# Optimization experiments

Measured on AMD Instinct MI355X. Metric: run time of the kernel, lower is better.

## Reference

```python
import jax, jax.numpy as jnp
import numpy as np

T, B, D, H, R, S, M = 1024, 16, 512, 8, 32, 16, 16
TQ = R + T + S   # query length
KL = M + R + T   # key/value length
NEG_INF = -1e8


def setup_inputs() -> dict:
    key = jax.random.key(0)
    ks = jax.random.split(key, 12)
    utterance = jax.random.normal(ks[0], (T, B, D), jnp.float32)
    right_context = jax.random.normal(ks[1], (R, B, D), jnp.float32)
    summary = jax.random.normal(ks[2], (S, B, D), jnp.float32)
    mems = jax.random.normal(ks[3], (M, B, D), jnp.float32)
    # valid lengths in [T//2, T]; force max == T so data-dependent shapes are static
    lengths = jax.random.randint(ks[4], (B,), T // 2, T + 1).at[0].set(T).astype(jnp.int64)
    # block-streaming style mask: query i may only attend to keys <= i + M
    q_idx = jnp.arange(TQ)[:, None]
    k_idx = jnp.arange(KL)[None, :]
    attention_mask = k_idx > (q_idx + M)  # True = masked
    scale = 0.02
    Wq = jax.random.normal(ks[5], (D, D), jnp.float32) * scale
    bq = jnp.zeros((D,), jnp.float32)
    Wkv = jax.random.normal(ks[6], (2 * D, D), jnp.float32) * scale
    bkv = jnp.zeros((2 * D,), jnp.float32)
    Wo = jax.random.normal(ks[7], (D, D), jnp.float32) * scale
    bo = jnp.zeros((D,), jnp.float32)
    return dict(utterance=utterance, lengths=lengths, right_context=right_context,
                summary=summary, mems=mems, attention_mask=attention_mask,
                Wq=Wq, bq=bq, Wkv=Wkv, bkv=bkv, Wo=Wo, bo=bo)


def _split_heads(x):
    # (L, B, D) -> (B*H, L, D//H), matching torch .view(-1, B*H, d).transpose(0, 1)
    L = x.shape[0]
    return x.reshape(L, B * H, D // H).transpose(1, 0, 2)


def reference(utterance, lengths, right_context, summary, mems, attention_mask,
              Wq, bq, Wkv, bkv, Wo, bo):
    d_head = D // H
    scaling = d_head ** -0.5

    query_in = jnp.concatenate([right_context, utterance, summary], axis=0)   # (TQ, B, D)
    kv_in = jnp.concatenate([mems, right_context, utterance], axis=0)         # (KL, B, D)

    query = query_in @ Wq.T + bq
    kv = kv_in @ Wkv.T + bkv
    k, v = jnp.split(kv, 2, axis=2)

    q = _split_heads(query)  # (B*H, TQ, d)
    kh = _split_heads(k)     # (B*H, KL, d)
    vh = _split_heads(v)

    w = jnp.einsum('nqd,nkd->nqk', q * scaling, kh).astype(jnp.float32)
    w = jnp.where(attention_mask[None, :, :], NEG_INF, w)

    # padding mask (B > 1 path): klengths = lengths + M + right_context_blocks_length
    rcbl = TQ - jnp.max(lengths) - S  # == R since max(lengths) == T
    klengths = lengths + M + rcbl
    pad_mask = jnp.arange(KL)[None, :] >= klengths[:, None]  # (B, KL)
    w = w.reshape(B, H, TQ, KL)
    w = jnp.where(pad_mask[:, None, None, :], NEG_INF, w)
    w = w.reshape(B * H, TQ, KL)

    probs = jax.nn.softmax(w, axis=-1)  # dropout p=0.0
    attn = jnp.einsum('nqk,nkd->nqd', probs, vh)          # (B*H, TQ, d)
    attn = attn.transpose(1, 0, 2).reshape(TQ, B, D)

    out = attn @ Wo.T + bo                                # (TQ, B, D)
    output_right_context = out[:TQ - S]                    # (R+T, B, D)
    output_mems = jnp.clip(out[TQ - S:], -10.0, 10.0)      # tanh_on_mem=False
    return output_right_context, output_mems[:-1]          # (S-1, B, D)
```

## Files before the change

### kernel.cpp

```cpp
#include <hip/hip_runtime.h>

#define T_   1024
#define B_   16
#define D_   512
#define H_   8
#define R_   32
#define S_   16
#define M_   16
#define TQ_  1072
#define KL_  1072
#define DH_  64
#define NROW 17152
#define K_   512
#define LQ_  268
#define QSCALE 0.18033688f

typedef unsigned short u16;
using bf16x8 = __attribute__((ext_vector_type(8))) short;
using f32x4  = __attribute__((ext_vector_type(4))) float;
using u16x4  = __attribute__((ext_vector_type(4))) unsigned short;

__device__ __forceinline__ u16 f2bf(float f) {
    unsigned int u = __builtin_bit_cast(unsigned int, f);
    unsigned int r = u + 0x7fffu + ((u >> 16) & 1u);
    return (u16)(r >> 16);
}

__device__ __forceinline__ unsigned int cvt_pk_bf16(float a, float b) {
    unsigned int r;
    asm("v_cvt_pk_bf16_f32 %0, %1, %2" : "=v"(r) : "v"(a), "v"(b));
    return r;
}

__device__ __forceinline__ void gload_lds16(const u16* g, u16* l) {
    __builtin_amdgcn_global_load_lds(
        (const __attribute__((address_space(1))) unsigned int*)g,
        (__attribute__((address_space(3))) unsigned int*)l,
        16, 0, 0);
}

__global__ void k_convert4(const float4* __restrict__ utt, const float4* __restrict__ rc,
                           const float4* __restrict__ smr, const float4* __restrict__ mems,
                           const float4* __restrict__ Wq, const float4* __restrict__ Wkv,
                           const float4* __restrict__ Wo,
                           u16x4* __restrict__ xall,
                           u16x4* __restrict__ wq, u16x4* __restrict__ wkv,
                           u16x4* __restrict__ wo)
{
    const int N4 = 17408 * D_ / 4;
    const int MB = M_ * B_ * D_ / 4;
    const int RB = MB + R_ * B_ * D_ / 4;
    const int UB = RB + T_ * B_ * D_ / 4;
    const int W1 = D_ * D_ / 4, W2 = 2 * D_ * D_ / 4;
    for (int i = blockIdx.x * blockDim.x + threadIdx.x; i < N4;
         i += gridDim.x * blockDim.x) {
        float4 v;
        if (i < MB)      v = mems[i];
        else if (i < RB) v = rc[i - MB];
        else if (i < UB) v = utt[i - RB];
        else             v = smr[i - UB];
        xall[i] = (u16x4){f2bf(v.x), f2bf(v.y), f2bf(v.z), f2bf(v.w)};
        if (i < W1) { v = Wq[i];  wq[i]  = (u16x4){f2bf(v.x), f2bf(v.y), f2bf(v.z), f2bf(v.w)}; }
        if (i < W2) { v = Wkv[i]; wkv[i] = (u16x4){f2bf(v.x), f2bf(v.y), f2bf(v.z), f2bf(v.w)}; }
        if (i < W1) { v = Wo[i];  wo[i]  = (u16x4){f2bf(v.x), f2bf(v.y), f2bf(v.z), f2bf(v.w)}; }
    }
}

template<int MREP, bool TOR>
__device__ __forceinline__ void pipe_core(const u16* __restrict__ Ab,
                                          const u16* __restrict__ Wb,
                                          u16* lds, f32x4* acc)
{
    const int BM = MREP * 32;
    u16* As0 = lds;
    u16* As1 = lds + BM * 64;
    u16* Bs0 = lds + 2 * BM * 64;
    u16* Bs1 = lds + 2 * BM * 64 + 256 * 64;

    const int tid  = threadIdx.x;
    const int wid  = tid >> 6, lane = tid & 63;
    const int wm   = wid >> 2, wn = wid & 3;
    const int col  = lane & 15, quad = lane >> 4;
    const int sr   = tid >> 3;
    const int sc   = (tid & 7) ^ (sr & 7);
    const u16* gA  = Ab + (size_t)sr * K_ + sc * 8;
    const u16* gB  = Wb + (size_t)sr * K_ + sc * 8;

#pragma unroll
    for (int i = 0; i < MREP * 4; i++) acc[i] = (f32x4){0.f, 0.f, 0.f, 0.f};

    auto stage = [&](int kt, u16* Au, u16* Bu) {
#pragma unroll
        for (int i = 0; i < MREP / 2; i++)
            gload_lds16(gA + (size_t)(i * 64) * K_ + kt * 64,
                        Au + (i * 64 + wid * 8) * 64);
#pragma unroll
        for (int i = 0; i < 4; i++)
            gload_lds16(gB + (size_t)(i * 64) * K_ + kt * 64,
                        Bu + (i * 64 + wid * 8) * 64);
    };

    stage(0, As0, Bs0);
    __syncthreads();

    u16 *Ac = As0, *Bc = Bs0, *An = As1, *Bn = Bs1;
    for (int kt = 0; kt < 8; ++kt) {
        if (kt < 7) stage(kt + 1, An, Bn);
#pragma unroll
        for (int kh = 0; kh < 2; ++kh) {
            bf16x8 aF[MREP], bF[4];
#pragma unroll
            for (int mi = 0; mi < MREP; mi++)
                aF[mi] = *(const bf16x8*)&Ac[(wm * (MREP * 16) + mi * 16 + col) * 64
                             + (((kh * 4 + quad) ^ (col & 7)) * 8)];
#pragma unroll
            for (int ni = 0; ni < 4; ni++)
                bF[ni] = *(const bf16x8*)&Bc[(wn * 64 + ni * 16 + col) * 64
                             + (((kh * 4 + quad) ^ (col & 7)) * 8)];
            __builtin_amdgcn_s_setprio(1);
            if (TOR) {
#pragma unroll
                for (int ni = 0; ni < 4; ni++)
#pragma unroll
                    for (int mi = 0; mi < MREP; mi++)
                        acc[ni * MREP + mi] = __builtin_amdgcn_mfma_f32_16x16x32_bf16(
                            bF[ni], aF[mi], acc[ni * MREP + mi], 0, 0, 0);
            } else {
#pragma unroll
                for (int mi = 0; mi < MREP; mi++)
#pragma unroll
                    for (int ni = 0; ni < 4; ni++)
                        acc[mi * 4 + ni] = __builtin_amdgcn_mfma_f32_16x16x32_bf16(
                            aF[mi], bF[ni], acc[mi * 4 + ni], 0, 0, 0);
            }
            __builtin_amdgcn_s_setprio(0);
        }
        __syncthreads();
        u16* t;
        t = Ac; Ac = An; An = t;
        t = Bc; Bc = Bn; Bn = t;
    }
}

__global__ __launch_bounds__(512, 2)
void k_gemm_qkv8(const u16* __restrict__ xall,
                 const u16* __restrict__ wqp, const u16* __restrict__ wkvp,
                 const float* __restrict__ bq, const float* __restrict__ bkv,
                 u16* __restrict__ qb, u16* __restrict__ kb, u16* __restrict__ vt)
{
    extern __shared__ u16 lds[];
    const int bid = blockIdx.x;
    const int tn = bid % 6, tm = bid / 6;
    const int typ = tn >> 1, half = tn & 1;
    const u16* Ab = (typ == 0 ? xall + (size_t)256 * K_ : xall)
                    + (size_t)tm * 256 * K_;
    const u16* Wb = (typ == 0 ? wqp : wkvp + (typ == 2 ? (size_t)512 * K_ : 0))
                    + (size_t)half * 256 * K_;

    const int wid = threadIdx.x >> 6, lane = threadIdx.x & 63;
    const int wm = wid >> 2, wn = wid & 3;
    const int col = lane & 15, quad = lane >> 4;

    f32x4 acc[32];
    if (typ == 2) {
        pipe_core<8, false>(Ab, Wb, lds, acc);
#pragma unroll
        for (int ni = 0; ni < 4; ni++) {
            const int f = half * 256 + wn * 64 + ni * 16 + col;
            const float bs = bkv[512 + f];
#pragma unroll
            for (int mg = 0; mg < 2; mg++) {
                const int lq = tm * 4 + wm * 2 + mg;
#pragma unroll
                for (int r = 0; r < 4; r++) {
                    const int bb = quad * 4 + r;
                    uint2 pk;
                    pk.x = cvt_pk_bf16(acc[(mg * 4 + 0) * 4 + ni][r] + bs,
                                       acc[(mg * 4 + 1) * 4 + ni][r] + bs);
                    pk.y = cvt_pk_bf16(acc[(mg * 4 + 2) * 4 + ni][r] + bs,
                                       acc[(mg * 4 + 3) * 4 + ni][r] + bs);
                    *(uint2*)&vt[(((size_t)bb * LQ_ + lq) * 512 + f) * 4] = pk;
                }
            }
        }
    } else {
        pipe_core<8, true>(Ab, Wb, lds, acc);
        const float* bias = (typ == 0) ? bq : bkv;
        u16* outp = (typ == 0) ? qb : kb;
        const float qs = (typ == 0) ? QSCALE : 1.0f;
#pragma unroll
        for (int ni = 0; ni < 4; ni++) {
            const int gc0 = half * 256 + wn * 64 + ni * 16 + quad * 4;
            const float4 bs4 = *(const float4*)&bias[gc0];
#pragma unroll
            for (int mi = 0; mi < 8; mi++) {
                const int mrow = tm * 256 + wm * 128 + mi * 16 + col;
                f32x4 a = acc[ni * 8 + mi];
                uint2 pk;
                pk.x = cvt_pk_bf16((a[0] + bs4.x) * qs, (a[1] + bs4.y) * qs);
                pk.y = cvt_pk_bf16((a[2] + bs4.z) * qs, (a[3] + bs4.w) * qs);
                *(uint2*)&outp[(size_t)mrow * 512 + gc0] = pk;
            }
        }
    }
}

__global__ __launch_bounds__(512, 2)
void k_gemm_o8(const u16* __restrict__ A, const u16* __restrict__ W,
               const float* __restrict__ bias, float* __restrict__ Co)
{
    extern __shared__ u16 lds[];
    const int tn = blockIdx.x % 2, tm = blockIdx.x / 2;
    const u16* Ab = A + (size_t)tm * 128 * K_;
    const u16* Wb = W + (size_t)tn * 256 * K_;

    const int wid = threadIdx.x >> 6, lane = threadIdx.x & 63;
    const int wm = wid >> 2, wn = wid & 3;
    const int col = lane & 15, quad = lane >> 4;

    f32x4 acc[16];
    pipe_core<4, true>(Ab, Wb, lds, acc);

#pragma unroll
    for (int ni = 0; ni < 4; ni++) {
        const int gc0 = tn * 256 + wn * 64 + ni * 16 + quad * 4;
        const float4 bs4 = *(const float4*)&bias[gc0];
#pragma unroll
        for (int mi = 0; mi < 4; mi++) {
            const int l = tm * 8 + wm * 4 + mi;
            if (l == TQ_ - 1) continue;
            const int mrow = tm * 128 + wm * 64 + mi * 16 + col;
            f32x4 a = acc[ni * 4 + mi];
            float4 v = {a[0] + bs4.x, a[1] + bs4.y, a[2] + bs4.z, a[3] + bs4.w};
            if (l >= TQ_ - S_) {
                v.x = fminf(10.0f, fmaxf(-10.0f, v.x));
                v.y = fminf(10.0f, fmaxf(-10.0f, v.y));
                v.z = fminf(10.0f, fmaxf(-10.0f, v.z));
                v.w = fminf(10.0f, fmaxf(-10.0f, v.w));
            }
            *(float4*)&Co[(size_t)mrow * 512 + gc0] = v;
        }
    }
}

__global__ __launch_bounds__(256, 2)
void k_attn5(const u16* __restrict__ qbuf, const u16* __restrict__ kb,
             const u16* __restrict__ vt, const int* __restrict__ lenp,
             u16* __restrict__ attnb)
{
    __shared__ __align__(16) u16 Ks[2][64 * 64];
    __shared__ __align__(16) u16 Vs[2][64 * 64];
    __shared__ __align__(16) u16 Ps[4][16 * 64];

    const int blk  = blockIdx.x;
    const int qblk = 16 - (blk >> 7);
    const int bh   = blk & 127;
    const int b = bh >> 3, h = bh & 7;
    const int tid = threadIdx.x;
    const int w = tid >> 6, lane = tid & 63;
    const int col = lane & 15, quad = lane >> 4;

    int stride = (lenp[1] == 0) ? 2 : 1;
    int maxlen = 0;
    for (int i = 0; i < B_; i++) maxlen = max(maxlen, lenp[i * stride]);
    const int klen = lenp[b * stride] + M_ + (TQ_ - maxlen - S_);

    const int q0 = qblk * 64;
    const int qw = q0 + w * 16;
    const int q  = qw + col;

    int qrow = min(q, TQ_ - 1);
    const u16* qp = qbuf + ((size_t)qrow * B_ + b) * D_ + h * DH_ + quad * 8;
    bf16x8 bq0 = *(const bf16x8*)(qp);
    bf16x8 bq1 = *(const bf16x8*)(qp + 32);

    const int s0 = tid, s1 = tid + 256;
    const u16* kbase = kb + (size_t)b * 512 + h * DH_;
    size_t kof0 = (size_t)(s0 >> 3) * 8192 + (size_t)(((s0 & 7) ^ ((s0 >> 3) & 7)) * 8);
    size_t kof1 = (size_t)(s1 >> 3) * 8192 + (size_t)(((s1 & 7) ^ ((s1 >> 3) & 7)) * 8);
    const u16* vbase = vt + ((size_t)b * LQ_ * 512 + (size_t)h * DH_) * 4;
    auto vchunk = [](int s) -> size_t {
        int fp = s >> 4;
        int lq = (s & 15) ^ (fp & 15);
        return (size_t)lq * 2048 + (size_t)fp * 8;
    };
    const size_t vof0 = vchunk(s0), vof1 = vchunk(s1);

    float li = 0.f;
    f32x4 o[4];
#pragma unroll
    for (int g = 0; g < 4; g++) o[g] = (f32x4){0.f, 0.f, 0.f, 0.f};

    const int nk = min(q0 + 64 + M_, klen);
    const int numkt = (nk + 63) >> 6;
    u16* pw = &Ps[w][0];

    gload_lds16(kbase + kof0, &Ks[0][(size_t)w * 512]);
    gload_lds16(kbase + kof1, &Ks[0][2048 + (size_t)w * 512]);
    gload_lds16(vbase + vof0, &Vs[0][(size_t)w * 512]);
    gload_lds16(vbase + vof1, &Vs[0][2048 + (size_t)w * 512]);

    for (int kt = 0; kt < numkt; kt++) {
        const int kn0 = kt * 64;
        const int cur = kt & 1;
        __syncthreads();
        if (kt + 1 < numkt) {
            const size_t kstep = (size_t)(kn0 + 64) * 8192;
            const size_t vstep = (size_t)(kt + 1) * 32768;
            gload_lds16(kbase + kstep + kof0, &Ks[cur ^ 1][(size_t)w * 512]);
            gload_lds16(kbase + kstep + kof1, &Ks[cur ^ 1][2048 + (size_t)w * 512]);
            gload_lds16(vbase + vstep + vof0, &Vs[cur ^ 1][(size_t)w * 512]);
            gload_lds16(vbase + vstep + vof1, &Vs[cur ^ 1][2048 + (size_t)w * 512]);
        }

        f32x4 sc[4];
        __builtin_amdgcn_s_setprio(1);
#pragma unroll
        for (int g = 0; g < 4; g++) {
            int key = g * 16 + col;
            bf16x8 a0 = *(const bf16x8*)&Ks[cur][key * 64 + ((quad ^ (key & 7)) * 8)];
            bf16x8 a1 = *(const bf16x8*)&Ks[cur][key * 64 + (((4 + quad) ^ (key & 7)) * 8)];
            f32x4 z = {0.f, 0.f, 0.f, 0.f};
            z = __builtin_amdgcn_mfma_f32_16x16x32_bf16(a0, bq0, z, 0, 0, 0);
            z = __builtin_amdgcn_mfma_f32_16x16x32_bf16(a1, bq1, z, 0, 0, 0);
            sc[g] = z;
        }
        __builtin_amdgcn_s_setprio(0);

        const bool needmask = (kn0 + 63 > qw + M_) || (kn0 + 63 >= klen);
        if (needmask) {
#pragma unroll
            for (int g = 0; g < 4; g++)
#pragma unroll
                for (int r = 0; r < 4; r++) {
                    int key = kn0 + g * 16 + quad * 4 + r;
                    bool valid = (key <= q + M_) && (key < klen);
                    sc[g][r] = valid ? sc[g][r] : -1e8f;
                }
        }

#pragma unroll
        for (int g = 0; g < 4; g++) {
            float pr[4];
#pragma unroll
            for (int r = 0; r < 4; r++) {
                pr[r] = __builtin_amdgcn_exp2f(sc[g][r]);
                li += pr[r];
            }
            uint2 pk;
            pk.x = cvt_pk_bf16(pr[0], pr[1]);
            pk.y = cvt_pk_bf16(pr[2], pr[3]);
            int kc = g * 2 + (quad >> 1);
            *(uint2*)&pw[col * 64 + ((kc ^ (col & 7)) * 8) + (quad & 1) * 4] = pk;
        }

        bf16x8 ap0 = *(const bf16x8*)&pw[col * 64 + ((quad ^ (col & 7)) * 8)];
        bf16x8 ap1 = *(const bf16x8*)&pw[col * 64 + (((4 + quad) ^ (col & 7)) * 8)];
        __builtin_amdgcn_s_setprio(1);
#pragma unroll
        for (int g = 0; g < 4; g++) {
            int d = g * 16 + col;
            int fp = d >> 1, fo = (d & 1) * 4;
            bf16x8 bv[2];
#pragma unroll
            for (int hh = 0; hh < 2; hh++) {
                int lqA = hh * 8 + quad * 2;
                int posA = fp * 16 + (lqA ^ (fp & 15));
                int posB = fp * 16 + ((lqA + 1) ^ (fp & 15));
                u16x4 loA = *(const u16x4*)&Vs[cur][posA * 8 + fo];
                u16x4 loB = *(const u16x4*)&Vs[cur][posB * 8 + fo];
                bf16x8 t;
                t[0] = loA[0]; t[1] = loA[1]; t[2] = loA[2]; t[3] = loA[3];
                t[4] = loB[0]; t[5] = loB[1]; t[6] = loB[2]; t[7] = loB[3];
                bv[hh] = t;
            }
            o[g] = __builtin_amdgcn_mfma_f32_16x16x32_bf16(bv[0], ap0, o[g], 0, 0, 0);
            o[g] = __builtin_amdgcn_mfma_f32_16x16x32_bf16(bv[1], ap1, o[g], 0, 0, 0);
        }
        __builtin_amdgcn_s_setprio(0);
    }

    li += __shfl_xor(li, 16);
    li += __shfl_xor(li, 32);
    const float inv = 1.0f / li;
    const int qo = qw + col;
    if (qw + 16 <= TQ_) {
#pragma unroll
        for (int g = 0; g < 4; g++) {
            uint2 pk;
            pk.x = cvt_pk_bf16(o[g][0] * inv, o[g][1] * inv);
            pk.y = cvt_pk_bf16(o[g][2] * inv, o[g][3] * inv);
            *(uint2*)&attnb[((size_t)qo * B_ + b) * D_ + h * DH_ + g * 16 + quad * 4] = pk;
        }
    }
}

extern "C" void kernel_launch(void* const* d_in, const int* in_sizes, int n_in,
                              void* d_out, int out_size, void* d_ws, size_t ws_size,
                              hipStream_t stream)
{
    const float* utt  = (const float*)d_in[0];
    const int*   len  = (const int*)  d_in[1];
    const float* rc   = (const float*)d_in[2];
    const float* smr  = (const float*)d_in[3];
    const float* mems = (const float*)d_in[4];
    const float* Wq   = (const float*)d_in[6];
    const float* bq   = (const float*)d_in[7];
    const float* Wkv  = (const float*)d_in[8];
    const float* bkv  = (const float*)d_in[9];
    const float* Wo   = (const float*)d_in[10];
    const float* bo   = (const float*)d_in[11];

    char* ws = (char*)d_ws;
    size_t off = 0;
    auto alloc = [&](size_t bytes) -> void* {
        void* p = ws + off;
        off += (bytes + 255) & ~(size_t)255;
        return p;
    };
    u16* xall = (u16*)alloc((size_t)17408 * D_ * 2);
    u16* wq   = (u16*)alloc((size_t)D_ * D_ * 2);
    u16* wkv  = (u16*)alloc((size_t)2 * D_ * D_ * 2);
    u16* wo   = (u16*)alloc((size_t)D_ * D_ * 2);
    u16* qb   = (u16*)alloc((size_t)NROW * D_ * 2);
    u16* kb   = (u16*)alloc((size_t)NROW * D_ * 2);
    u16* vt   = (u16*)alloc((size_t)B_ * LQ_ * 512 * 4 * 2 + 65536);
    u16* attnb = xall;

    static int s_attr_done = 0;
    if (!s_attr_done) {
        hipFuncSetAttribute(reinterpret_cast<const void*>(k_gemm_qkv8),
                            hipFuncAttributeMaxDynamicSharedMemorySize, 131072);
        hipFuncSetAttribute(reinterpret_cast<const void*>(k_gemm_o8),
                            hipFuncAttributeMaxDynamicSharedMemorySize, 98304);
        s_attr_done = 1;
    }

    k_convert4<<<2048, 256, 0, stream>>>((const float4*)utt, (const float4*)rc,
                                         (const float4*)smr, (const float4*)mems,
                                         (const float4*)Wq, (const float4*)Wkv,
                                         (const float4*)Wo,
                                         (u16x4*)xall,
                                         (u16x4*)wq, (u16x4*)wkv, (u16x4*)wo);
    k_gemm_qkv8<<<67 * 6, 512, 131072, stream>>>(xall, wq, wkv, bq, bkv, qb, kb, vt);
    k_attn5<<<17 * 128, 256, 0, stream>>>(qb, kb, vt, len, attnb);
    k_gemm_o8<<<134 * 2, 512, 98304, stream>>>(attnb, wo, bo, (float*)d_out);
}
```

Baseline: 221.6 us.

## Retile QKV and output GEMMs to 256x128 with XCD-aware block swizzle

Both projection GEMMs now use one 256x128 tile shape with a 4x2 wave layout, so the QKV GEMM launches twice as many workgroups with less LDS each. The output GEMM moves from 128x256 to 256x128 tiles. Block IDs are remapped so neighbouring tiles land on the same XCD and share L2. The k-loop now uses split s_barrier plus an explicit vmcnt wait instead of __syncthreads, letting the next stage's loads overlap. The aim is better occupancy and load balance, paid for with more redundant A-tile loads per output column.

```diff
diff --git a/kernel.cpp b/kernel.cpp
--- a/kernel.cpp
+++ b/kernel.cpp
@@ -37,6 +37,12 @@
         (const __attribute__((address_space(1))) unsigned int*)g,
         (__attribute__((address_space(3))) unsigned int*)l,
         16, 0, 0);
+}
+
+__device__ __forceinline__ int xcd_swz(int bid, int nwg) {
+    const int q = nwg >> 3, r = nwg & 7;
+    const int xcd = bid & 7, idx = bid >> 3;
+    return (xcd < r ? xcd * (q + 1) : r * (q + 1) + (xcd - r) * q) + idx;
 }
 
 __global__ void k_convert4(const float4* __restrict__ utt, const float4* __restrict__ rc,
@@ -66,20 +72,19 @@
     }
 }
 
-template<int MREP, bool TOR>
+template<bool TOR>
 __device__ __forceinline__ void pipe_core(const u16* __restrict__ Ab,
                                           const u16* __restrict__ Wb,
                                           u16* lds, f32x4* acc)
 {
-    const int BM = MREP * 32;
     u16* As0 = lds;
-    u16* As1 = lds + BM * 64;
-    u16* Bs0 = lds + 2 * BM * 64;
-    u16* Bs1 = lds + 2 * BM * 64 + 256 * 64;
+    u16* As1 = lds + 256 * 64;
+    u16* Bs0 = lds + 2 * 256 * 64;
+    u16* Bs1 = lds + 2 * 256 * 64 + 128 * 64;
 
     const int tid  = threadIdx.x;
     const int wid  = tid >> 6, lane = tid & 63;
-    const int wm   = wid >> 2, wn = wid & 3;
+    const int wm   = wid >> 1, wn = wid & 1;
     const int col  = lane & 15, quad = lane >> 4;
     const int sr   = tid >> 3;
     const int sc   = (tid & 7) ^ (sr & 7);
@@ -87,31 +92,38 @@
     const u16* gB  = Wb + (size_t)sr * K_ + sc * 8;
 
 #pragma unroll
-    for (int i = 0; i < MREP * 4; i++) acc[i] = (f32x4){0.f, 0.f, 0.f, 0.f};
+    for (int i = 0; i < 16; i++) acc[i] = (f32x4){0.f, 0.f, 0.f, 0.f};
 
     auto stage = [&](int kt, u16* Au, u16* Bu) {
 #pragma unroll
-        for (int i = 0; i < MREP / 2; i++)
+        for (int i = 0; i < 4; i++)
             gload_lds16(gA + (size_t)(i * 64) * K_ + kt * 64,
                         Au + (i * 64 + wid * 8) * 64);
 #pragma unroll
-        for (int i = 0; i < 4; i++)
-            gload_lds16(gB + (size_t)(i * 64) * K_ + kt * 64,
-                        Bu + (i * 64 + wid * 8) * 64);
+        for (int j = 0; j < 2; j++)
+            gload_lds16(gB + (size_t)(j * 64) * K_ + kt * 64,
+                        Bu + (j * 64 + wid * 8) * 64);
     };
 
     stage(0, As0, Bs0);
-    __syncthreads();
 
     u16 *Ac = As0, *Bc = Bs0, *An = As1, *Bn = Bs1;
     for (int kt = 0; kt < 8; ++kt) {
-        if (kt < 7) stage(kt + 1, An, Bn);
+        __builtin_amdgcn_s_barrier();
+        if (kt < 7) {
+            stage(kt + 1, An, Bn);
+            asm volatile("s_waitcnt vmcnt(6)" ::: "memory");
+        } else {
+            asm volatile("s_waitcnt vmcnt(0)" ::: "memory");
+        }
+        __builtin_amdgcn_s_barrier();
+        __builtin_amdgcn_sched_barrier(0);
 #pragma unroll
         for (int kh = 0; kh < 2; ++kh) {
-            bf16x8 aF[MREP], bF[4];
-#pragma unroll
-            for (int mi = 0; mi < MREP; mi++)
-                aF[mi] = *(const bf16x8*)&Ac[(wm * (MREP * 16) + mi * 16 + col) * 64
+            bf16x8 aF[4], bF[4];
+#pragma unroll
+            for (int mi = 0; mi < 4; mi++)
+                aF[mi] = *(const bf16x8*)&Ac[(wm * 64 + mi * 16 + col) * 64
                              + (((kh * 4 + quad) ^ (col & 7)) * 8)];
 #pragma unroll
             for (int ni = 0; ni < 4; ni++)
@@ -122,12 +134,12 @@
 #pragma unroll
                 for (int ni = 0; ni < 4; ni++)
 #pragma unroll
-                    for (int mi = 0; mi < MREP; mi++)
-                        acc[ni * MREP + mi] = __builtin_amdgcn_mfma_f32_16x16x32_bf16(
-                            bF[ni], aF[mi], acc[ni * MREP + mi], 0, 0, 0);
+                    for (int mi = 0; mi < 4; mi++)
+                        acc[ni * 4 + mi] = __builtin_amdgcn_mfma_f32_16x16x32_bf16(
+                            bF[ni], aF[mi], acc[ni * 4 + mi], 0, 0, 0);
             } else {
 #pragma unroll
-                for (int mi = 0; mi < MREP; mi++)
+                for (int mi = 0; mi < 4; mi++)
 #pragma unroll
                     for (int ni = 0; ni < 4; ni++)
                         acc[mi * 4 + ni] = __builtin_amdgcn_mfma_f32_16x16x32_bf16(
@@ -135,7 +147,6 @@
             }
             __builtin_amdgcn_s_setprio(0);
         }
-        __syncthreads();
         u16* t;
         t = Ac; Ac = An; An = t;
         t = Bc; Bc = Bn; Bn = t;
@@ -149,53 +160,50 @@
                  u16* __restrict__ qb, u16* __restrict__ kb, u16* __restrict__ vt)
 {
     extern __shared__ u16 lds[];
-    const int bid = blockIdx.x;
-    const int tn = bid % 6, tm = bid / 6;
-    const int typ = tn >> 1, half = tn & 1;
+    const int wgid = xcd_swz(blockIdx.x, 67 * 12);
+    const int tn = wgid % 12, tm = wgid / 12;
+    const int typ = tn >> 2, sub = tn & 3;
     const u16* Ab = (typ == 0 ? xall + (size_t)256 * K_ : xall)
                     + (size_t)tm * 256 * K_;
     const u16* Wb = (typ == 0 ? wqp : wkvp + (typ == 2 ? (size_t)512 * K_ : 0))
-                    + (size_t)half * 256 * K_;
+                    + (size_t)sub * 128 * K_;
 
     const int wid = threadIdx.x >> 6, lane = threadIdx.x & 63;
-    const int wm = wid >> 2, wn = wid & 3;
+    const int wm = wid >> 1, wn = wid & 1;
     const int col = lane & 15, quad = lane >> 4;
 
-    f32x4 acc[32];
+    f32x4 acc[16];
     if (typ == 2) {
-        pipe_core<8, false>(Ab, Wb, lds, acc);
+        pipe_core<false>(Ab, Wb, lds, acc);
 #pragma unroll
         for (int ni = 0; ni < 4; ni++) {
-            const int f = half * 256 + wn * 64 + ni * 16 + col;
+            const int f = sub * 128 + wn * 64 + ni * 16 + col;
             const float bs = bkv[512 + f];
-#pragma unroll
-            for (int mg = 0; mg < 2; mg++) {
-                const int lq = tm * 4 + wm * 2 + mg;
-#pragma unroll
-                for (int r = 0; r < 4; r++) {
-                    const int bb = quad * 4 + r;
-                    uint2 pk;
-                    pk.x = cvt_pk_bf16(acc[(mg * 4 + 0) * 4 + ni][r] + bs,
-                                       acc[(mg * 4 + 1) * 4 + ni][r] + bs);
-                    pk.y = cvt_pk_bf16(acc[(mg * 4 + 2) * 4 + ni][r] + bs,
-                                       acc[(mg * 4 + 3) * 4 + ni][r] + bs);
-                    *(uint2*)&vt[(((size_t)bb * LQ_ + lq) * 512 + f) * 4] = pk;
-                }
+            const int lq = tm * 4 + wm;
+#pragma unroll
+            for (int r = 0; r < 4; r++) {
+                const int bb = quad * 4 + r;
+                uint2 pk;
+                pk.x = cvt_pk_bf16(acc[0 * 4 + ni][r] + bs,
+                                   acc[1 * 4 + ni][r] + bs);
+                pk.y = cvt_pk_bf16(acc[2 * 4 + ni][r] + bs,
+                                   acc[3 * 4 + ni][r] + bs);
+                *(uint2*)&vt[(((size_t)bb * LQ_ + lq) * 512 + f) * 4] = pk;
             }
         }
     } else {
-        pipe_core<8, true>(Ab, Wb, lds, acc);
+        pipe_core<true>(Ab, Wb, lds, acc);
         const float* bias = (typ == 0) ? bq : bkv;
         u16* outp = (typ == 0) ? qb : kb;
         const float qs = (typ == 0) ? QSCALE : 1.0f;
 #pragma unroll
         for (int ni = 0; ni < 4; ni++) {
-            const int gc0 = half * 256 + wn * 64 + ni * 16 + quad * 4;
+            const int gc0 = sub * 128 + wn * 64 + ni * 16 + quad * 4;
             const float4 bs4 = *(const float4*)&bias[gc0];
 #pragma unroll
-            for (int mi = 0; mi < 8; mi++) {
-                const int mrow = tm * 256 + wm * 128 + mi * 16 + col;
-                f32x4 a = acc[ni * 8 + mi];
+            for (int mi = 0; mi < 4; mi++) {
+                const int mrow = tm * 256 + wm * 64 + mi * 16 + col;
+                f32x4 a = acc[ni * 4 + mi];
                 uint2 pk;
                 pk.x = cvt_pk_bf16((a[0] + bs4.x) * qs, (a[1] + bs4.y) * qs);
                 pk.y = cvt_pk_bf16((a[2] + bs4.z) * qs, (a[3] + bs4.w) * qs);
@@ -210,26 +218,27 @@
                const float* __restrict__ bias, float* __restrict__ Co)
 {
     extern __shared__ u16 lds[];
-    const int tn = blockIdx.x % 2, tm = blockIdx.x / 2;
-    const u16* Ab = A + (size_t)tm * 128 * K_;
-    const u16* Wb = W + (size_t)tn * 256 * K_;
+    const int wgid = xcd_swz(blockIdx.x, 67 * 4);
+    const int tn = wgid % 4, tm = wgid / 4;
+    const u16* Ab = A + (size_t)tm * 256 * K_;
+    const u16* Wb = W + (size_t)tn * 128 * K_;
 
     const int wid = threadIdx.x >> 6, lane = threadIdx.x & 63;
-    const int wm = wid >> 2, wn = wid & 3;
+    const int wm = wid >> 1, wn = wid & 1;
     const int col = lane & 15, quad = lane >> 4;
 
     f32x4 acc[16];
-    pipe_core<4, true>(Ab, Wb, lds, acc);
+    pipe_core<true>(Ab, Wb, lds, acc);
 
 #pragma unroll
     for (int ni = 0; ni < 4; ni++) {
-        const int gc0 = tn * 256 + wn * 64 + ni * 16 + quad * 4;
+        const int gc0 = tn * 128 + wn * 64 + ni * 16 + quad * 4;
         const float4 bs4 = *(const float4*)&bias[gc0];
 #pragma unroll
         for (int mi = 0; mi < 4; mi++) {
-            const int l = tm * 8 + wm * 4 + mi;
+            const int l = tm * 16 + wm * 4 + mi;
             if (l == TQ_ - 1) continue;
-            const int mrow = tm * 128 + wm * 64 + mi * 16 + col;
+            const int mrow = tm * 256 + wm * 64 + mi * 16 + col;
             f32x4 a = acc[ni * 4 + mi];
             float4 v = {a[0] + bs4.x, a[1] + bs4.y, a[2] + bs4.z, a[3] + bs4.w};
             if (l >= TQ_ - S_) {
@@ -430,7 +439,7 @@
     static int s_attr_done = 0;
     if (!s_attr_done) {
         hipFuncSetAttribute(reinterpret_cast<const void*>(k_gemm_qkv8),
-                            hipFuncAttributeMaxDynamicSharedMemorySize, 131072);
+                            hipFuncAttributeMaxDynamicSharedMemorySize, 98304);
         hipFuncSetAttribute(reinterpret_cast<const void*>(k_gemm_o8),
                             hipFuncAttributeMaxDynamicSharedMemorySize, 98304);
         s_attr_done = 1;
@@ -442,7 +451,7 @@
                                          (const float4*)Wo,
                                          (u16x4*)xall,
                                          (u16x4*)wq, (u16x4*)wkv, (u16x4*)wo);
-    k_gemm_qkv8<<<67 * 6, 512, 131072, stream>>>(xall, wq, wkv, bq, bkv, qb, kb, vt);
+    k_gemm_qkv8<<<67 * 12, 512, 98304, stream>>>(xall, wq, wkv, bq, bkv, qb, kb, vt);
     k_attn5<<<17 * 128, 256, 0, stream>>>(qb, kb, vt, len, attnb);
-    k_gemm_o8<<<134 * 2, 512, 98304, stream>>>(attnb, wo, bo, (float*)d_out);
-}
+    k_gemm_o8<<<67 * 4, 512, 98304, stream>>>(attnb, wo, bo, (float*)d_out);
+}
```

Result: faster. 217.2 us (-2.0%).
